# Optimization experiments

Hardware: AMD Instinct MI355X
Metric: run time of the kernel (lower is better)

Reference implementation:

```python
import jax, jax.numpy as jnp
import numpy as np

B, S, D, H = 4, 1024, 1024, 16
HD = D // H  # per-head dim = 64
NEG = -10000000000.0


def setup_inputs() -> dict:
    key = jax.random.key(0)
    ks = jax.random.split(key, 12)
    q = jax.random.normal(ks[0], (B, S, D), jnp.float32)
    k = jax.random.normal(ks[1], (B, S, D), jnp.float32)
    v = jax.random.normal(ks[2], (B, S, D), jnp.float32)
    mask = jax.random.randint(ks[3], (B, S, S), 0, 2).astype(jnp.int32)
    sc = 1.0 / np.sqrt(D)
    Wq = jax.random.normal(ks[4], (H, D, HD), jnp.float32) * sc
    bq = jnp.zeros((H, HD), jnp.float32)
    Wk = jax.random.normal(ks[5], (H, D, HD), jnp.float32) * sc
    bk = jnp.zeros((H, HD), jnp.float32)
    Wv = jax.random.normal(ks[6], (H, D, HD), jnp.float32) * sc
    bv = jnp.zeros((H, HD), jnp.float32)
    Wo = jax.random.normal(ks[7], (D, D), jnp.float32) * sc
    bo = jnp.zeros((D,), jnp.float32)
    return {"query": q, "key": k, "value": v, "attention_mask": mask,
            "Wq": Wq, "bq": bq, "Wk": Wk, "bk": bk, "Wv": Wv, "bv": bv,
            "Wo": Wo, "bo": bo}


def reference(query, key, value, attention_mask, Wq, bq, Wk, bk, Wv, bv, Wo, bo):
    # batched per-head projections: [B,S,D] x [H,D,E] -> [B,H,S,E]
    q = jnp.einsum('bsd,hde->bhse', query, Wq) + bq[None, :, None, :]
    k = jnp.einsum('bsd,hde->bhse', key, Wk) + bk[None, :, None, :]
    v = jnp.einsum('bsd,hde->bhse', value, Wv) + bv[None, :, None, :]
    # NOTE: scale uses key_dim (model_size = full D), faithful to source
    score = jnp.einsum('bhse,bhte->bhst', q, k) / jnp.sqrt(jnp.float32(D))
    m = attention_mask.astype(jnp.float32)[:, None, :, :]  # [B,1,S,S]
    score = score + (1.0 - m) * NEG
    attn = jax.nn.softmax(score, axis=-1) * m  # double masking
    heads = jnp.einsum('bhst,bhte->bhse', attn, v)  # [B,H,S,E]
    # concat heads along feature dim (head order preserved)
    heads = heads.transpose(0, 2, 1, 3).reshape(B, S, D)
    return heads @ Wo + bo
```

## Files before the change

kernel.cpp:

```cpp
#include <hip/hip_runtime.h>

#define B_ 4
#define S_ 1024
#define D_ 1024
#define H_ 16
#define E_ 64
#define BS_ (B_*S_)
#define BHSE_ (B_*H_*S_*E_)

typedef __attribute__((ext_vector_type(8))) short bf16x8;
typedef __attribute__((ext_vector_type(4))) float f32x4;
typedef __attribute__((ext_vector_type(4))) unsigned int u32x4;

__device__ __forceinline__ unsigned short f2bf(float f) {
    unsigned int x = __float_as_uint(f);
    x = (x + 0x7FFFu + ((x >> 16) & 1u)) >> 16;
    return (unsigned short)x;
}
__device__ __forceinline__ float bf2f(unsigned short u) {
    return __uint_as_float(((unsigned int)u) << 16);
}
__device__ __forceinline__ float ldin(const void* p, size_t i, int isb) {
    return isb ? bf2f(((const unsigned short*)p)[i]) : ((const float*)p)[i];
}

__device__ __forceinline__ unsigned int cvtpk(float lo, float hi) {
    unsigned int r;
    asm("v_cvt_pk_bf16_f32 %0, %1, %2" : "=v"(r) : "v"(lo), "v"(hi));
    return r;
}
__device__ __forceinline__ unsigned int bperm(int srclane4, unsigned int v) {
    return (unsigned int)__builtin_amdgcn_ds_bpermute(srclane4, (int)v);
}
__device__ __forceinline__ bf16x8 u4bf(u32x4 w) {
    union { u32x4 u; bf16x8 h; } c; c.u = w; return c.h;
}

#if __has_builtin(__builtin_amdgcn_exp2f)
#define EXP2(x) __builtin_amdgcn_exp2f(x)
#else
#define EXP2(x) __expf((x) * 0.6931471805599453f)
#endif

__device__ __forceinline__ void gl2lds16(const void* g, void* l) {
    __builtin_amdgcn_global_load_lds(
        (const __attribute__((address_space(1))) void*)g,
        (__attribute__((address_space(3))) void*)l, 16, 0, 0);
}

__device__ __forceinline__ int detect_isb(const unsigned int* q) {
    unsigned int wv = q[threadIdx.x & 63];
    unsigned int lo = wv & 0xFFFFu;
    unsigned int e = (lo >> 7) & 0xFFu;
    int ok = (lo == 0u) || (e >= 100u && e <= 145u);
    return __popcll(__ballot(ok)) >= 48;
}

__global__ __launch_bounds__(256) void preproc(
        const void* q_, const void* k_, const void* v_, const int* mask,
        const void* Wq, const void* Wk, const void* Wv, const void* Wo,
        const void* bq_, const void* bk_, const void* bv_, const void* bo_,
        unsigned short* WT, float* biases, unsigned long long* packT,
        unsigned short* Aconv) {
    __shared__ unsigned short Tt[64][72];
    const int isb = detect_isb((const unsigned int*)q_);
    const int blk = blockIdx.x, t = threadIdx.x;

    if (blk < 1024) {
        const int c0 = blk & 15, r0 = ((blk >> 4) & 15) * 64, z = blk >> 8;
        const void* src = (z == 0) ? Wq : (z == 1) ? Wk : (z == 2) ? Wv : Wo;
        {
            int dl = t >> 2, qc = t & 3;
            size_t base;
            if (z < 3) base = (size_t)c0 * 65536 + (size_t)(r0 + dl) * 64 + qc * 16;
            else       base = (size_t)(r0 + dl) * 1024 + (size_t)c0 * 64 + qc * 16;
            if (isb) {
                const unsigned short* s = (const unsigned short*)src + base;
                bf16x8 a0 = *(const bf16x8*)s, a1 = *(const bf16x8*)(s + 8);
#pragma unroll
                for (int j = 0; j < 8; j++) {
                    Tt[qc * 16 + j][dl] = (unsigned short)a0[j];
                    Tt[qc * 16 + 8 + j][dl] = (unsigned short)a1[j];
                }
            } else {
                const float* s = (const float*)src + base;
#pragma unroll
                for (int j = 0; j < 16; j++) Tt[qc * 16 + j][dl] = f2bf(s[j]);
            }
        }
        __syncthreads();
        {
            int el = t >> 2, qc = t & 3;
            size_t dst = (size_t)z * D_ * D_ + (size_t)(c0 * 64 + el) * D_ + r0 + qc * 16;
            *(bf16x8*)&WT[dst]     = *(const bf16x8*)&Tt[el][qc * 16];
            *(bf16x8*)&WT[dst + 8] = *(const bf16x8*)&Tt[el][qc * 16 + 8];
        }
        if (z == 3 && ((blk >> 4) & 15) == 0 && c0 < 4) {
            const void* bs = (c0 == 0) ? bq_ : (c0 == 1) ? bk_
                           : (c0 == 2) ? bv_ : bo_;
#pragma unroll
            for (int j = 0; j < 4; j++) {
                int i = t * 4 + j;
                biases[c0 * 1024 + i] = ldin(bs, i, isb);
            }
        }
    } else if (blk < 5120) {
        int unit = (blk - 1024) * 4 + (t >> 6);
        int lane = t & 63;
        int b = unit >> 12, rem = unit & 4095, s0 = (rem >> 4) * 4, kt = rem & 15;
        const int* mb = mask + ((size_t)b * 1024 + s0) * 1024 + kt * 64 + lane;
        unsigned long long bits[4];
#pragma unroll
        for (int j = 0; j < 4; j++) bits[j] = __ballot(mb[j * 1024] != 0);
        if (lane < 4) {
            unsigned long long bb = (lane == 0) ? bits[0] : (lane == 1) ? bits[1]
                                  : (lane == 2) ? bits[2] : bits[3];
            packT[((size_t)b * 16 + kt) * 1024 + s0 + lane] = bb;
        }
    } else {
        if (isb) return;
        int blk2 = blk - 5120;
        const int z = blk2 >> 11;
        const float* s = (z == 0) ? (const float*)q_ : (z == 1) ? (const float*)k_
                                                                : (const float*)v_;
        const size_t i = ((size_t)(blk2 & 2047) * 256 + t) * 8;
        f32x4 a0 = *(const f32x4*)(s + i);
        f32x4 a1 = *(const f32x4*)(s + i + 4);
        bf16x8 o;
#pragma unroll
        for (int j = 0; j < 4; j++) {
            o[j]     = (short)f2bf(a0[j]);
            o[4 + j] = (short)f2bf(a1[j]);
        }
        *(bf16x8*)&Aconv[(size_t)z * ((size_t)BS_ * D_) + i] = o;
    }
}

template<int BM, int BN, int MODE, int MINW>
__global__ __launch_bounds__(256, MINW) void gemm_k(
        const void* A0, const void* A1, const void* A2, const unsigned short* Aconv,
        const unsigned short* BtB, const float* biasB, void* dstB,
        const unsigned int* qdet) {
    constexpr int TOT16 = (BM + BN) * 32;
    constexpr int CALLS = TOT16 / 512;
    constexpr int CPW = CALLS / 4;
    constexpr int MT = BM / 32;
    constexpr int NT = BN / 32;
    __shared__ unsigned short buf[3][TOT16];

    const int fl = detect_isb(qdet);
    const int t = threadIdx.x, lane = t & 63, w = t >> 6;
    const int lm = lane & 15, q4 = lane >> 4;
    const int wm = w >> 1, wn = w & 1;
    const int lr = lane >> 2;
    const int ls = lane & 3;
    const int lg = ls ^ ((lr >> 1) & 3);

    const unsigned short* Abf;
    const unsigned short* Bt;
    const float* bias;
    int z = 0, m0, n0, phase;
    if (MODE == 0) {
        int bid = blockIdx.x + gridDim.x * (blockIdx.y + gridDim.y * blockIdx.z);
        int xcd = bid & 7, idx = bid >> 3;
        z = idx >> 5;
        int r = idx & 31;
        int mt = (xcd << 2) + (r & 3);
        int nt = r >> 2;
        m0 = mt * BM; n0 = nt * BN;
        phase = (nt * 13 + z * 5) & 31;
        const void* Ain = (z == 0) ? A0 : (z == 1 ? A1 : A2);
        Abf = fl ? (const unsigned short*)Ain
                 : Aconv + (size_t)z * ((size_t)BS_ * D_);
        Bt = BtB + (size_t)z * D_ * D_;
        bias = biasB + z * 1024;
    } else {
        Abf = (const unsigned short*)A0;
        Bt = BtB; bias = biasB;
        int bid = blockIdx.x + (blockIdx.y << 5);
        int xcd = bid & 7, idx = bid >> 3;
        m0 = ((xcd << 2) + (idx & 3)) * BM;
        n0 = (idx >> 2) * BN;
        phase = ((idx >> 2) * 13) & 31;
    }

    auto stage = [&](int kk, int bi) {
#pragma unroll
        for (int i = 0; i < CPW; ++i) {
            int c = w * CPW + i;
            int row = c * 16 + lr;
            const unsigned short* g;
            if (row < BM)
                g = Abf + (size_t)(m0 + row) * D_ + kk + lg * 8;
            else
                g = Bt + (size_t)(n0 + row - BM) * D_ + kk + lg * 8;
            gl2lds16(g, &buf[bi][c * 512]);
        }
    };

    f32x4 acc[MT][NT];
#pragma unroll
    for (int i = 0; i < MT; i++)
#pragma unroll
        for (int j = 0; j < NT; j++) acc[i][j] = (f32x4){0.f, 0.f, 0.f, 0.f};

    stage((phase & 31) * 32, 0);
    stage(((1 + phase) & 31) * 32, 1);
    for (int it = 0; it < D_ / 32; ++it) {
        const int bi = it % 3;
        if (it < D_ / 32 - 1) {
            asm volatile("s_waitcnt vmcnt(%0)" :: "n"(CPW) : "memory");
        } else {
            asm volatile("s_waitcnt vmcnt(0)" ::: "memory");
        }
        __builtin_amdgcn_s_barrier();
        __builtin_amdgcn_sched_barrier(0);
        if (it < D_ / 32 - 2) stage(((it + 2 + phase) & 31) * 32, (it + 2) % 3);

        const unsigned short* As = buf[bi];
        const unsigned short* Bs = buf[bi] + BM * 32;
        bf16x8 af[MT], bv[NT];
#pragma unroll
        for (int mt = 0; mt < MT; mt++) {
            int row = wm * (BM / 2) + mt * 16 + lm;
            af[mt] = *(const bf16x8*)&As[row * 32 + (q4 ^ ((row >> 1) & 3)) * 8];
        }
#pragma unroll
        for (int nt = 0; nt < NT; nt++) {
            int row = wn * (BN / 2) + nt * 16 + lm;
            bv[nt] = *(const bf16x8*)&Bs[row * 32 + (q4 ^ ((row >> 1) & 3)) * 8];
        }
#pragma unroll
        for (int mt = 0; mt < MT; mt++)
#pragma unroll
            for (int nt = 0; nt < NT; nt++)
                acc[mt][nt] = __builtin_amdgcn_mfma_f32_16x16x32_bf16(
                    af[mt], bv[nt], acc[mt][nt], 0, 0, 0);
    }

#pragma unroll
    for (int mt = 0; mt < MT; mt++)
#pragma unroll
        for (int nt = 0; nt < NT; nt++) {
            int N = n0 + wn * (BN / 2) + nt * 16 + lm;
            int Mb = m0 + wm * (BM / 2) + mt * 16 + q4 * 4;
            if (MODE == 0 && z == 2) {
                int bb = Mb >> 10, sb = Mb & 1023, hh = N >> 6, e = N & 63;
                unsigned long long hv = 0;
#pragma unroll
                for (int r = 0; r < 4; r++)
                    hv |= (unsigned long long)f2bf(acc[mt][nt][r] + bias[N]) << (16 * r);
                unsigned short* d16 = (unsigned short*)dstB + (size_t)2 * BHSE_;
                *(unsigned long long*)&d16[(((size_t)(bb * H_ + hh) * E_ + e) << 10) + sb] = hv;
            } else {
#pragma unroll
                for (int r = 0; r < 4; r++) {
                    int M = Mb + r;
                    float v = acc[mt][nt][r] + bias[N];
                    if (MODE == 0) {
                        int bb = M >> 10, s = M & 1023, hh = N >> 6, e = N & 63;
                        unsigned short* d16 = (unsigned short*)dstB + (size_t)z * BHSE_;
                        d16[((size_t)(bb * H_ + hh) * S_ + s) * E_ + e] = f2bf(v);
                    } else {
                        size_t idx = (size_t)M * D_ + N;
                        if (fl) ((unsigned short*)dstB)[idx] = f2bf(v);
                        else    ((float*)dstB)[idx] = v;
                    }
                }
            }
        }
}

__global__ __launch_bounds__(1024, 4) void attn64(
        const unsigned short* Qp, const unsigned short* Kp, const unsigned short* VpT,
        const unsigned long long* packT, unsigned short* heads) {
    __shared__ unsigned short KT[2][8192];
    __shared__ unsigned short VT[2][8192];

    const int bid = blockIdx.x + (blockIdx.y << 2) + (blockIdx.z << 6);
    const int xcd = bid & 7, idx = bid >> 3;
    const int qt = idx >> 3;
    const int hb = xcd * 8 + (idx & 7);
    const int h = hb & 15, b = hb >> 4;

    const int t = threadIdx.x, w = t >> 6, lane = t & 63, lm = lane & 15, q4 = lane >> 4;
    const size_t bh = ((size_t)b * H_ + h) * S_ * E_;
    const unsigned short* Qb = Qp + bh;
    const unsigned short* Kb = Kp + bh;
    const unsigned short* Vb = VpT + bh;
    const int q0 = qt * 256 + w * 16;

    const int l3 = lane >> 3, l7 = lane & 7;
    const int kLaneOff = l3 * 64 + (l7 ^ l3) * 8;
    const int vLaneOff = l3 * 1024 + (l7 ^ l3) * 8;

    const int sw = lm & 7;
    const int c0 = (q4 ^ sw) * 8, c1 = ((q4 ^ 4) ^ sw) * 8;

    const int srcA4 = ((lane & 15) | ((lane & 16) << 1)) << 2;
    const int srcB4 = srcA4 + 64;
    const bool selHi = (lane & 32) != 0;

    bf16x8 bq0 = *(const bf16x8*)&Qb[(size_t)(q0 + lm) * E_ + q4 * 8];
    bf16x8 bq1 = *(const bf16x8*)&Qb[(size_t)(q0 + lm) * E_ + 32 + q4 * 8];

    bf16x8 ones;
#pragma unroll
    for (int j = 0; j < 8; j++) ones[j] = (short)0x3F80;

    f32x4 oacc[4];
#pragma unroll
    for (int i = 0; i < 4; i++) oacc[i] = (f32x4){0.f, 0.f, 0.f, 0.f};
    f32x4 accL = (f32x4){0.f, 0.f, 0.f, 0.f};
    float mrun = -3.0e38f;
    const float scale2 = 0.03125f * 1.4426950408889634f;

#define STAGE(tile, bufi)                                                     \
    {                                                                         \
        int k0s = (tile) * 128;                                               \
        _Pragma("unroll")                                                     \
        for (int i_ = 0; i_ < 2; ++i_) {                                      \
            int c_ = w * 2 + i_;                                              \
            if (c_ < 16) {                                                    \
                gl2lds16(Kb + (size_t)k0s * 64 + c_ * 512 + kLaneOff,         \
                         &KT[bufi][c_ * 512]);                                \
            } else {                                                          \
                int cc_ = c_ - 16, sub_ = cc_ >> 3, ec_ = cc_ & 7;            \
                gl2lds16(Vb + (size_t)ec_ * 8192 + k0s + sub_ * 64 + vLaneOff,\
                         &VT[bufi][sub_ * 4096 + ec_ * 512]);                 \
            }                                                                 \
        }                                                                     \
    }

    STAGE(0, 0)
    unsigned long long mk0 = packT[(size_t)b * 16 * 1024 + q0 + lm];
    unsigned long long mk1 = packT[((size_t)b * 16 + 1) * 1024 + q0 + lm];

    for (int T = 0; T < S_ / 128; ++T) {
        const int bufi = T & 1;
        __syncthreads();
        unsigned long long mkn0 = 0, mkn1 = 0;
        if (T < 7) {
            STAGE(T + 1, bufi ^ 1)
            mkn0 = packT[((size_t)b * 16 + 2 * T + 2) * 1024 + q0 + lm];
            mkn1 = packT[((size_t)b * 16 + 2 * T + 3) * 1024 + q0 + lm];
        }

        f32x4 st[2][4];
#pragma unroll
        for (int sub = 0; sub < 2; ++sub)
#pragma unroll
            for (int jt = 0; jt < 4; ++jt) {
                const unsigned short* kr = &KT[bufi][(sub * 64 + jt * 16 + lm) * 64];
                bf16x8 ka0 = *(const bf16x8*)&kr[c0];
                bf16x8 ka1 = *(const bf16x8*)&kr[c1];
                f32x4 zz = (f32x4){0.f, 0.f, 0.f, 0.f};
                zz = __builtin_amdgcn_mfma_f32_16x16x32_bf16(ka0, bq0, zz, 0, 0, 0);
                zz = __builtin_amdgcn_mfma_f32_16x16x32_bf16(ka1, bq1, zz, 0, 0, 0);
                st[sub][jt] = zz;
            }

        float tmx = -3.0e38f;
#pragma unroll
        for (int sub = 0; sub < 2; ++sub)
#pragma unroll
            for (int jt = 0; jt < 4; ++jt) {
                float a = fmaxf(st[sub][jt][0], st[sub][jt][1]);
                float c = fmaxf(st[sub][jt][2], st[sub][jt][3]);
                tmx = fmaxf(tmx, fmaxf(a, c));
            }
        float pmax = tmx * scale2;

        if (!__all(pmax - mrun <= 8.f)) {
            float rmx = pmax;
            rmx = fmaxf(rmx, __shfl_xor(rmx, 16, 64));
            rmx = fmaxf(rmx, __shfl_xor(rmx, 32, 64));
            float mnew = fmaxf(mrun, rmx);
            float alpha = EXP2(mrun - mnew);
            accL = accL * alpha;
#pragma unroll
            for (int nt = 0; nt < 4; nt++) oacc[nt] = oacc[nt] * alpha;
            mrun = mnew;
        }
        const float mneg = -mrun;

        unsigned int cl[2][8];
#pragma unroll
        for (int sub = 0; sub < 2; ++sub) {
            unsigned long long mk = sub ? mk1 : mk0;
            unsigned int mn = (unsigned int)(mk >> (q4 * 4));
            unsigned int mh = (unsigned int)(mk >> (q4 * 4 + 32));
#pragma unroll
            for (int jt = 0; jt < 4; ++jt) {
                unsigned int mm = (jt & 2) ? mh : mn;
                const int sh = (jt & 1) * 16;
                float p0 = EXP2(fmaf(st[sub][jt][0], scale2, mneg));
                float p1 = EXP2(fmaf(st[sub][jt][1], scale2, mneg));
                float p2 = EXP2(fmaf(st[sub][jt][2], scale2, mneg));
                float p3 = EXP2(fmaf(st[sub][jt][3], scale2, mneg));
                p0 = (mm & (1u << (sh + 0))) ? p0 : 0.f;
                p1 = (mm & (1u << (sh + 1))) ? p1 : 0.f;
                p2 = (mm & (1u << (sh + 2))) ? p2 : 0.f;
                p3 = (mm & (1u << (sh + 3))) ? p3 : 0.f;
                cl[sub][jt * 2]     = cvtpk(p0, p1);
                cl[sub][jt * 2 + 1] = cvtpk(p2, p3);
            }
        }

#pragma unroll
        for (int sub = 0; sub < 2; ++sub) {
            unsigned int* c = cl[sub];
            u32x4 w0, w1;
            {
                unsigned int aA0 = bperm(srcA4, c[0]), aA2 = bperm(srcA4, c[2]);
                unsigned int aA1 = bperm(srcA4, c[1]), aA3 = bperm(srcA4, c[3]);
                unsigned int aB0 = bperm(srcB4, c[0]), aB2 = bperm(srcB4, c[2]);
                unsigned int aB1 = bperm(srcB4, c[1]), aB3 = bperm(srcB4, c[3]);
                w0 = (u32x4){selHi ? aA2 : aA0, selHi ? aA3 : aA1,
                             selHi ? aB2 : aB0, selHi ? aB3 : aB1};
                unsigned int bA0 = bperm(srcA4, c[4]), bA2 = bperm(srcA4, c[6]);
                unsigned int bA1 = bperm(srcA4, c[5]), bA3 = bperm(srcA4, c[7]);
                unsigned int bB0 = bperm(srcB4, c[4]), bB2 = bperm(srcB4, c[6]);
                unsigned int bB1 = bperm(srcB4, c[5]), bB3 = bperm(srcB4, c[7]);
                w1 = (u32x4){selHi ? bA2 : bA0, selHi ? bA3 : bA1,
                             selHi ? bB2 : bB0, selHi ? bB3 : bB1};
            }
            bf16x8 bp0 = u4bf(w0);
            bf16x8 bp1 = u4bf(w1);

            accL = __builtin_amdgcn_mfma_f32_16x16x32_bf16(ones, bp0, accL, 0, 0, 0);
            accL = __builtin_amdgcn_mfma_f32_16x16x32_bf16(ones, bp1, accL, 0, 0, 0);

            const unsigned short* vbase = &VT[bufi][sub * 4096];
#pragma unroll
            for (int nt = 0; nt < 4; nt++) {
                const unsigned short* vr = &vbase[(nt * 16 + lm) * 64];
                bf16x8 va0 = *(const bf16x8*)&vr[c0];
                bf16x8 va1 = *(const bf16x8*)&vr[c1];
                oacc[nt] = __builtin_amdgcn_mfma_f32_16x16x32_bf16(va0, bp0, oacc[nt], 0, 0, 0);
                oacc[nt] = __builtin_amdgcn_mfma_f32_16x16x32_bf16(va1, bp1, oacc[nt], 0, 0, 0);
            }
        }

        mk0 = mkn0; mk1 = mkn1;
    }

    float inv = 1.0f / accL[0];
#pragma unroll
    for (int nt = 0; nt < 4; nt++) {
        unsigned int lo = cvtpk(oacc[nt][0] * inv, oacc[nt][1] * inv);
        unsigned int hi = cvtpk(oacc[nt][2] * inv, oacc[nt][3] * inv);
        unsigned long long hv = (unsigned long long)lo | ((unsigned long long)hi << 32);
        *(unsigned long long*)&heads[(size_t)(b * S_ + q0 + lm) * D_ + h * E_ + nt * 16 + q4 * 4] = hv;
    }
}

extern "C" void kernel_launch(void* const* d_in, const int* in_sizes, int n_in,
                              void* d_out, int out_size, void* d_ws, size_t ws_size,
                              hipStream_t stream) {
    char* ws = (char*)d_ws;
    unsigned short* WT = (unsigned short*)(ws + 256);
    unsigned short* WqT = WT;
    unsigned short* WoT = WT + (size_t)3 * D_ * D_;
    float* biases = (float*)(WT + (size_t)4 * D_ * D_);
    float* bq = biases;
    float* bo = biases + 3 * 1024;
    unsigned short* Qp = (unsigned short*)(biases + 4 * 1024);
    unsigned short* Kp = Qp + (size_t)BHSE_;
    unsigned short* Vp = Kp + (size_t)BHSE_;
    unsigned short* heads = Vp + (size_t)BHSE_;
    unsigned long long* packT = (unsigned long long*)(heads + (size_t)BHSE_);
    unsigned short* Aconv = (unsigned short*)(packT + (size_t)B_ * 16 * S_);

    preproc<<<11264, 256, 0, stream>>>(
        d_in[0], d_in[1], d_in[2], (const int*)d_in[3],
        d_in[4], d_in[6], d_in[8], d_in[10],
        d_in[5], d_in[7], d_in[9], d_in[11],
        WT, biases, packT, Aconv);
    gemm_k<128, 128, 0, 3><<<dim3(32, 8, 3), 256, 0, stream>>>(
        d_in[0], d_in[1], d_in[2], Aconv, WqT, bq, Qp,
        (const unsigned int*)d_in[0]);
    attn64<<<dim3(4, 16, 4), 1024, 0, stream>>>(Qp, Kp, Vp, packT, heads);
    gemm_k<128, 64, 1, 4><<<dim3(32, 16, 1), 256, 0, stream>>>(
        heads, nullptr, nullptr, nullptr, WoT, bo, d_out,
        (const unsigned int*)d_in[0]);
}
```

Measured before the change: 224.5 us.

## Double attention KV tile to 256 keys and raise wave priority around MFMA

The attention kernel now stages 256 keys per iteration into doubled K/V shared-memory buffers, and processes each tile as two 128-key halves. This halves the number of loop iterations and block barriers and prefetches four mask words at a time. It also brackets the MFMA sections with s_setprio so the matrix work gets issue priority. The cost is that shared memory per block doubles to about 128 KB, which likely allows fewer resident blocks per CU and so less latency hiding.

```diff
diff --git a/kernel.cpp b/kernel.cpp
--- a/kernel.cpp
+++ b/kernel.cpp
@@ -274,8 +274,8 @@
 __global__ __launch_bounds__(1024, 4) void attn64(
         const unsigned short* Qp, const unsigned short* Kp, const unsigned short* VpT,
         const unsigned long long* packT, unsigned short* heads) {
-    __shared__ unsigned short KT[2][8192];
-    __shared__ unsigned short VT[2][8192];
+    __shared__ unsigned short KT[2][16384];
+    __shared__ unsigned short VT[2][16384];
 
     const int bid = blockIdx.x + (blockIdx.y << 2) + (blockIdx.z << 6);
     const int xcd = bid & 7, idx = bid >> 3;
@@ -317,15 +317,15 @@
 
 #define STAGE(tile, bufi)                                                     \
     {                                                                         \
-        int k0s = (tile) * 128;                                               \
+        int k0s = (tile) * 256;                                               \
         _Pragma("unroll")                                                     \
-        for (int i_ = 0; i_ < 2; ++i_) {                                      \
-            int c_ = w * 2 + i_;                                              \
-            if (c_ < 16) {                                                    \
+        for (int i_ = 0; i_ < 4; ++i_) {                                      \
+            int c_ = w * 4 + i_;                                              \
+            if (c_ < 32) {                                                    \
                 gl2lds16(Kb + (size_t)k0s * 64 + c_ * 512 + kLaneOff,         \
                          &KT[bufi][c_ * 512]);                                \
             } else {                                                          \
-                int cc_ = c_ - 16, sub_ = cc_ >> 3, ec_ = cc_ & 7;            \
+                int cc_ = c_ - 32, sub_ = cc_ >> 3, ec_ = cc_ & 7;            \
                 gl2lds16(Vb + (size_t)ec_ * 8192 + k0s + sub_ * 64 + vLaneOff,\
                          &VT[bufi][sub_ * 4096 + ec_ * 512]);                 \
             }                                                                 \
@@ -333,116 +333,127 @@
     }
 
     STAGE(0, 0)
-    unsigned long long mk0 = packT[(size_t)b * 16 * 1024 + q0 + lm];
-    unsigned long long mk1 = packT[((size_t)b * 16 + 1) * 1024 + q0 + lm];
-
-    for (int T = 0; T < S_ / 128; ++T) {
+    unsigned long long mk[4], mkn[4];
+#pragma unroll
+    for (int j = 0; j < 4; j++)
+        mk[j] = packT[((size_t)b * 16 + j) * 1024 + q0 + lm];
+
+    for (int T = 0; T < S_ / 256; ++T) {
         const int bufi = T & 1;
         __syncthreads();
-        unsigned long long mkn0 = 0, mkn1 = 0;
-        if (T < 7) {
+        if (T < 3) {
             STAGE(T + 1, bufi ^ 1)
-            mkn0 = packT[((size_t)b * 16 + 2 * T + 2) * 1024 + q0 + lm];
-            mkn1 = packT[((size_t)b * 16 + 2 * T + 3) * 1024 + q0 + lm];
-        }
-
-        f32x4 st[2][4];
-#pragma unroll
-        for (int sub = 0; sub < 2; ++sub)
-#pragma unroll
-            for (int jt = 0; jt < 4; ++jt) {
-                const unsigned short* kr = &KT[bufi][(sub * 64 + jt * 16 + lm) * 64];
-                bf16x8 ka0 = *(const bf16x8*)&kr[c0];
-                bf16x8 ka1 = *(const bf16x8*)&kr[c1];
-                f32x4 zz = (f32x4){0.f, 0.f, 0.f, 0.f};
-                zz = __builtin_amdgcn_mfma_f32_16x16x32_bf16(ka0, bq0, zz, 0, 0, 0);
-                zz = __builtin_amdgcn_mfma_f32_16x16x32_bf16(ka1, bq1, zz, 0, 0, 0);
-                st[sub][jt] = zz;
-            }
-
-        float tmx = -3.0e38f;
-#pragma unroll
-        for (int sub = 0; sub < 2; ++sub)
-#pragma unroll
-            for (int jt = 0; jt < 4; ++jt) {
-                float a = fmaxf(st[sub][jt][0], st[sub][jt][1]);
-                float c = fmaxf(st[sub][jt][2], st[sub][jt][3]);
-                tmx = fmaxf(tmx, fmaxf(a, c));
-            }
-        float pmax = tmx * scale2;
-
-        if (!__all(pmax - mrun <= 8.f)) {
-            float rmx = pmax;
-            rmx = fmaxf(rmx, __shfl_xor(rmx, 16, 64));
-            rmx = fmaxf(rmx, __shfl_xor(rmx, 32, 64));
-            float mnew = fmaxf(mrun, rmx);
-            float alpha = EXP2(mrun - mnew);
-            accL = accL * alpha;
-#pragma unroll
-            for (int nt = 0; nt < 4; nt++) oacc[nt] = oacc[nt] * alpha;
-            mrun = mnew;
-        }
-        const float mneg = -mrun;
-
-        unsigned int cl[2][8];
-#pragma unroll
-        for (int sub = 0; sub < 2; ++sub) {
-            unsigned long long mk = sub ? mk1 : mk0;
-            unsigned int mn = (unsigned int)(mk >> (q4 * 4));
-            unsigned int mh = (unsigned int)(mk >> (q4 * 4 + 32));
-#pragma unroll
-            for (int jt = 0; jt < 4; ++jt) {
-                unsigned int mm = (jt & 2) ? mh : mn;
-                const int sh = (jt & 1) * 16;
-                float p0 = EXP2(fmaf(st[sub][jt][0], scale2, mneg));
-                float p1 = EXP2(fmaf(st[sub][jt][1], scale2, mneg));
-                float p2 = EXP2(fmaf(st[sub][jt][2], scale2, mneg));
-                float p3 = EXP2(fmaf(st[sub][jt][3], scale2, mneg));
-                p0 = (mm & (1u << (sh + 0))) ? p0 : 0.f;
-                p1 = (mm & (1u << (sh + 1))) ? p1 : 0.f;
-                p2 = (mm & (1u << (sh + 2))) ? p2 : 0.f;
-                p3 = (mm & (1u << (sh + 3))) ? p3 : 0.f;
-                cl[sub][jt * 2]     = cvtpk(p0, p1);
-                cl[sub][jt * 2 + 1] = cvtpk(p2, p3);
-            }
-        }
-
-#pragma unroll
-        for (int sub = 0; sub < 2; ++sub) {
-            unsigned int* c = cl[sub];
-            u32x4 w0, w1;
-            {
-                unsigned int aA0 = bperm(srcA4, c[0]), aA2 = bperm(srcA4, c[2]);
-                unsigned int aA1 = bperm(srcA4, c[1]), aA3 = bperm(srcA4, c[3]);
-                unsigned int aB0 = bperm(srcB4, c[0]), aB2 = bperm(srcB4, c[2]);
-                unsigned int aB1 = bperm(srcB4, c[1]), aB3 = bperm(srcB4, c[3]);
-                w0 = (u32x4){selHi ? aA2 : aA0, selHi ? aA3 : aA1,
-                             selHi ? aB2 : aB0, selHi ? aB3 : aB1};
-                unsigned int bA0 = bperm(srcA4, c[4]), bA2 = bperm(srcA4, c[6]);
-                unsigned int bA1 = bperm(srcA4, c[5]), bA3 = bperm(srcA4, c[7]);
-                unsigned int bB0 = bperm(srcB4, c[4]), bB2 = bperm(srcB4, c[6]);
-                unsigned int bB1 = bperm(srcB4, c[5]), bB3 = bperm(srcB4, c[7]);
-                w1 = (u32x4){selHi ? bA2 : bA0, selHi ? bA3 : bA1,
-                             selHi ? bB2 : bB0, selHi ? bB3 : bB1};
-            }
-            bf16x8 bp0 = u4bf(w0);
-            bf16x8 bp1 = u4bf(w1);
-
-            accL = __builtin_amdgcn_mfma_f32_16x16x32_bf16(ones, bp0, accL, 0, 0, 0);
-            accL = __builtin_amdgcn_mfma_f32_16x16x32_bf16(ones, bp1, accL, 0, 0, 0);
-
-            const unsigned short* vbase = &VT[bufi][sub * 4096];
-#pragma unroll
-            for (int nt = 0; nt < 4; nt++) {
-                const unsigned short* vr = &vbase[(nt * 16 + lm) * 64];
-                bf16x8 va0 = *(const bf16x8*)&vr[c0];
-                bf16x8 va1 = *(const bf16x8*)&vr[c1];
-                oacc[nt] = __builtin_amdgcn_mfma_f32_16x16x32_bf16(va0, bp0, oacc[nt], 0, 0, 0);
-                oacc[nt] = __builtin_amdgcn_mfma_f32_16x16x32_bf16(va1, bp1, oacc[nt], 0, 0, 0);
-            }
-        }
-
-        mk0 = mkn0; mk1 = mkn1;
+#pragma unroll
+            for (int j = 0; j < 4; j++)
+                mkn[j] = packT[((size_t)b * 16 + 4 * T + 4 + j) * 1024 + q0 + lm];
+        }
+
+#pragma unroll
+        for (int half = 0; half < 2; ++half) {
+            f32x4 st[2][4];
+            __builtin_amdgcn_s_setprio(1);
+#pragma unroll
+            for (int sub = 0; sub < 2; ++sub)
+#pragma unroll
+                for (int jt = 0; jt < 4; ++jt) {
+                    const unsigned short* kr =
+                        &KT[bufi][(half * 128 + sub * 64 + jt * 16 + lm) * 64];
+                    bf16x8 ka0 = *(const bf16x8*)&kr[c0];
+                    bf16x8 ka1 = *(const bf16x8*)&kr[c1];
+                    f32x4 zz = (f32x4){0.f, 0.f, 0.f, 0.f};
+                    zz = __builtin_amdgcn_mfma_f32_16x16x32_bf16(ka0, bq0, zz, 0, 0, 0);
+                    zz = __builtin_amdgcn_mfma_f32_16x16x32_bf16(ka1, bq1, zz, 0, 0, 0);
+                    st[sub][jt] = zz;
+                }
+            __builtin_amdgcn_s_setprio(0);
+
+            float tmx = -3.0e38f;
+#pragma unroll
+            for (int sub = 0; sub < 2; ++sub)
+#pragma unroll
+                for (int jt = 0; jt < 4; ++jt) {
+                    float a = fmaxf(st[sub][jt][0], st[sub][jt][1]);
+                    float c = fmaxf(st[sub][jt][2], st[sub][jt][3]);
+                    tmx = fmaxf(tmx, fmaxf(a, c));
+                }
+            float pmax = tmx * scale2;
+
+            if (!__all(pmax - mrun <= 8.f)) {
+                float rmx = pmax;
+                rmx = fmaxf(rmx, __shfl_xor(rmx, 16, 64));
+                rmx = fmaxf(rmx, __shfl_xor(rmx, 32, 64));
+                float mnew = fmaxf(mrun, rmx);
+                float alpha = EXP2(mrun - mnew);
+                accL = accL * alpha;
+#pragma unroll
+                for (int nt = 0; nt < 4; nt++) oacc[nt] = oacc[nt] * alpha;
+                mrun = mnew;
+            }
+            const float mneg = -mrun;
+
+            unsigned int cl[2][8];
+#pragma unroll
+            for (int sub = 0; sub < 2; ++sub) {
+                unsigned long long mkv = mk[half * 2 + sub];
+                unsigned int mn = (unsigned int)(mkv >> (q4 * 4));
+                unsigned int mh = (unsigned int)(mkv >> (q4 * 4 + 32));
+#pragma unroll
+                for (int jt = 0; jt < 4; ++jt) {
+                    unsigned int mm = (jt & 2) ? mh : mn;
+                    const int sh = (jt & 1) * 16;
+                    float p0 = EXP2(fmaf(st[sub][jt][0], scale2, mneg));
+                    float p1 = EXP2(fmaf(st[sub][jt][1], scale2, mneg));
+                    float p2 = EXP2(fmaf(st[sub][jt][2], scale2, mneg));
+                    float p3 = EXP2(fmaf(st[sub][jt][3], scale2, mneg));
+                    p0 = (mm & (1u << (sh + 0))) ? p0 : 0.f;
+                    p1 = (mm & (1u << (sh + 1))) ? p1 : 0.f;
+                    p2 = (mm & (1u << (sh + 2))) ? p2 : 0.f;
+                    p3 = (mm & (1u << (sh + 3))) ? p3 : 0.f;
+                    cl[sub][jt * 2]     = cvtpk(p0, p1);
+                    cl[sub][jt * 2 + 1] = cvtpk(p2, p3);
+                }
+            }
+
+#pragma unroll
+            for (int sub = 0; sub < 2; ++sub) {
+                unsigned int* c = cl[sub];
+                u32x4 w0, w1;
+                {
+                    unsigned int aA0 = bperm(srcA4, c[0]), aA2 = bperm(srcA4, c[2]);
+                    unsigned int aA1 = bperm(srcA4, c[1]), aA3 = bperm(srcA4, c[3]);
+                    unsigned int aB0 = bperm(srcB4, c[0]), aB2 = bperm(srcB4, c[2]);
+                    unsigned int aB1 = bperm(srcB4, c[1]), aB3 = bperm(srcB4, c[3]);
+                    w0 = (u32x4){selHi ? aA2 : aA0, selHi ? aA3 : aA1,
+                                 selHi ? aB2 : aB0, selHi ? aB3 : aB1};
+                    unsigned int bA0 = bperm(srcA4, c[4]), bA2 = bperm(srcA4, c[6]);
+                    unsigned int bA1 = bperm(srcA4, c[5]), bA3 = bperm(srcA4, c[7]);
+                    unsigned int bB0 = bperm(srcB4, c[4]), bB2 = bperm(srcB4, c[6]);
+                    unsigned int bB1 = bperm(srcB4, c[5]), bB3 = bperm(srcB4, c[7]);
+                    w1 = (u32x4){selHi ? bA2 : bA0, selHi ? bA3 : bA1,
+                                 selHi ? bB2 : bB0, selHi ? bB3 : bB1};
+                }
+                bf16x8 bp0 = u4bf(w0);
+                bf16x8 bp1 = u4bf(w1);
+
+                __builtin_amdgcn_s_setprio(1);
+                accL = __builtin_amdgcn_mfma_f32_16x16x32_bf16(ones, bp0, accL, 0, 0, 0);
+                accL = __builtin_amdgcn_mfma_f32_16x16x32_bf16(ones, bp1, accL, 0, 0, 0);
+
+                const unsigned short* vbase = &VT[bufi][(half * 2 + sub) * 4096];
+#pragma unroll
+                for (int nt = 0; nt < 4; nt++) {
+                    const unsigned short* vr = &vbase[(nt * 16 + lm) * 64];
+                    bf16x8 va0 = *(const bf16x8*)&vr[c0];
+                    bf16x8 va1 = *(const bf16x8*)&vr[c1];
+                    oacc[nt] = __builtin_amdgcn_mfma_f32_16x16x32_bf16(va0, bp0, oacc[nt], 0, 0, 0);
+                    oacc[nt] = __builtin_amdgcn_mfma_f32_16x16x32_bf16(va1, bp1, oacc[nt], 0, 0, 0);
+                }
+                __builtin_amdgcn_s_setprio(0);
+            }
+        }
+
+#pragma unroll
+        for (int j = 0; j < 4; j++) mk[j] = mkn[j];
     }
 
     float inv = 1.0f / accL[0];
```

After: 219.9 us, median of 2. 2.0% less time.
